# Kernel optimization log

Measured on AMD Instinct MI355X. Metric: run time of the kernel, lower is better.

The kernel has to match this reference:

```python
import jax, jax.numpy as jnp
import numpy as np

D_MODEL = 1024
D_HEAD = 64
B, S = 4, 4096


def setup_inputs() -> dict:
    key = jax.random.key(0)
    ks = jax.random.split(key, 7)
    inv = 1.0 / np.sqrt(D_MODEL)
    return {
        "x": jax.random.normal(ks[0], (B, S, D_MODEL), dtype=jnp.float32),
        "W_q": jax.random.normal(ks[1], (D_MODEL, D_HEAD), dtype=jnp.float32) * inv,
        "b_q": jax.random.normal(ks[2], (D_HEAD,), dtype=jnp.float32) * 0.02,
        "W_k": jax.random.normal(ks[3], (D_MODEL, D_HEAD), dtype=jnp.float32) * inv,
        "b_k": jax.random.normal(ks[4], (D_HEAD,), dtype=jnp.float32) * 0.02,
        "W_v": jax.random.normal(ks[5], (D_MODEL, D_HEAD), dtype=jnp.float32) * inv,
        "b_v": jax.random.normal(ks[6], (D_HEAD,), dtype=jnp.float32) * 0.02,
    }


def reference(x, W_q, b_q, W_k, b_k, W_v, b_v):
    # Projections: [B, S, d_head]
    Q = jnp.einsum("bsd,dh->bsh", x, W_q) + b_q
    K = jnp.einsum("bsd,dh->bsh", x, W_k) + b_k
    V = jnp.einsum("bsd,dh->bsh", x, W_v) + b_v
    scale = 1.0 / jnp.sqrt(jnp.asarray(Q.shape[-1], dtype=Q.dtype))
    scores = jnp.einsum("bqh,bkh->bqk", Q, K) * scale  # [B, S, S]
    seq_len = x.shape[1]
    causal = jnp.tril(jnp.ones((seq_len, seq_len), dtype=bool))
    scores = jnp.where(causal, scores, jnp.asarray(-jnp.inf, dtype=scores.dtype))
    A = jax.nn.softmax(scores, axis=-1)
    return jnp.einsum("bqk,bkh->bqh", A, V)  # [B, S, d_head]
```

## Files before the change

kernel.cpp:

```cpp
#include <hip/hip_runtime.h>

typedef __attribute__((ext_vector_type(4))) float f32x4;
typedef __attribute__((ext_vector_type(8))) short short8;
typedef unsigned short ushort_t;

constexpr int DM = 1024, DH = 64, S = 4096, B = 4;
constexpr float QSCALE = 0.125f * 1.44269504088896340736f;
constexpr int SPLIT = 4;

constexpr size_t WBT_OFF = 0;
constexpr size_t QB_OFF  = 393216;
constexpr size_t KB_OFF  = QB_OFF + 2097152;
constexpr size_t VT_OFF  = KB_OFF + 2097152;
constexpr size_t ML_OFF  = VT_OFF + 2097152;
constexpr size_t PO_OFF  = ML_OFF + 524288;

__device__ __forceinline__ ushort_t f2bf(float f) {
    unsigned u = __float_as_uint(f);
    u += 0x7FFFu + ((u >> 16) & 1u);
    return (ushort_t)(u >> 16);
}

__device__ __forceinline__ unsigned cvt_pk_bf16(float lo, float hi) {
    unsigned r;
    asm volatile("v_cvt_pk_bf16_f32 %0, %1, %2" : "=v"(r) : "v"(lo), "v"(hi));
    return r;
}

__device__ __forceinline__ void gl_lds16(const void* g, void* l) {
    __builtin_amdgcn_global_load_lds(
        (const __attribute__((address_space(1))) unsigned int*)g,
        (__attribute__((address_space(3))) unsigned int*)l, 16, 0, 0);
}

__global__ __launch_bounds__(256) void prep_w_kernel(
    const float* __restrict__ Wq, const float* __restrict__ Wk,
    const float* __restrict__ Wv, ushort_t* __restrict__ wbt)
{
    const int n = blockIdx.x;
    const int p = n >> 6, d = n & 63;
    const float* W = (p == 0) ? Wq : (p == 1) ? Wk : Wv;
    const int k0 = threadIdx.x * 4;
    ushort4 pack;
    pack.x = f2bf(W[(k0 + 0) * DH + d]);
    pack.y = f2bf(W[(k0 + 1) * DH + d]);
    pack.z = f2bf(W[(k0 + 2) * DH + d]);
    pack.w = f2bf(W[(k0 + 3) * DH + d]);
    *reinterpret_cast<ushort4*>(wbt + (size_t)n * DM + k0) = pack;
}

__global__ __launch_bounds__(512, 4) void qkv_mfma_kernel(
    const float* __restrict__ x, const ushort_t* __restrict__ wbt,
    const float* __restrict__ bq, const float* __restrict__ bk,
    const float* __restrict__ bv,
    ushort_t* __restrict__ qb, ushort_t* __restrict__ kb, ushort_t* __restrict__ vt)
{
    __shared__ uint4 AsU[2][256];
    __shared__ uint4 BsU[2][768];

    const int tid = threadIdx.x;
    const int wid = tid >> 6, lane = tid & 63;
    const int q16 = lane & 15, lg = lane >> 4;
    const int sub = wid & 1, np = wid >> 1;
    const int r0 = blockIdx.x * 32;
    const char* xB = (const char*)x;
    const char* wB = (const char*)wbt;

    auto task = [&](int tk, int buf, int kk) {
        if (tk < 4) {
            gl_lds16(xB + (size_t)(r0 + tk * 8 + (lane >> 3)) * 4096 + kk * 4
                        + (((lane & 7) ^ (lane >> 3)) << 4),
                     (char*)&AsU[buf][0] + tk * 1024 + lane * 16);
        } else {
            const int sg = tk - 4;
            gl_lds16(wB + (size_t)(sg * 16 + (lane >> 2)) * 2048 + kk * 2
                        + ((((lane & 3) ^ ((lane >> 2) & 3))) << 4),
                     (char*)&BsU[buf][0] + sg * 1024 + lane * 16);
        }
    };

    f32x4 acc[3];
#pragma unroll
    for (int j = 0; j < 3; ++j) acc[j] = {0.f, 0.f, 0.f, 0.f};

    task(2 * wid, 0, 0);
    task(2 * wid + 1, 0, 0);
    __syncthreads();

    const int row = sub * 16 + q16;
    for (int s = 0; s < 32; ++s) {
        const int buf = s & 1;
        if (s + 1 < 32) {
            task(2 * wid, buf ^ 1, (s + 1) * 32);
            task(2 * wid + 1, buf ^ 1, (s + 1) * 32);
        }
        const char* AsC = (const char*)&AsU[buf][0];
        const char* BsC = (const char*)&BsU[buf][0];
        const f32x4 a0 = *(const f32x4*)(AsC + row * 128 + (((2 * lg) ^ (row & 7)) << 4));
        const f32x4 a1 = *(const f32x4*)(AsC + row * 128 + (((2 * lg + 1) ^ (row & 7)) << 4));
        short8 Af;
        Af[0] = (short)f2bf(a0[0]); Af[1] = (short)f2bf(a0[1]);
        Af[2] = (short)f2bf(a0[2]); Af[3] = (short)f2bf(a0[3]);
        Af[4] = (short)f2bf(a1[0]); Af[5] = (short)f2bf(a1[1]);
        Af[6] = (short)f2bf(a1[2]); Af[7] = (short)f2bf(a1[3]);
        __builtin_amdgcn_s_setprio(1);
#pragma unroll
        for (int j = 0; j < 3; ++j) {
            const int nt = np * 3 + j;
            const short8 Bf = *(const short8*)(
                BsC + (nt * 16 + q16) * 64 + ((lg ^ (q16 & 3)) << 4));
            acc[j] = __builtin_amdgcn_mfma_f32_16x16x32_bf16(Af, Bf, acc[j], 0, 0, 0);
        }
        __builtin_amdgcn_s_setprio(0);
        __syncthreads();
    }

#pragma unroll
    for (int j = 0; j < 3; ++j) {
        const int nt = np * 3 + j;
        const int p = nt >> 2, d = ((nt & 3) << 4) + q16;
        const float* bp = (p == 0) ? bq : (p == 1) ? bk : bv;
        const float bb = bp[d];
#pragma unroll
        for (int r = 0; r < 4; ++r) {
            const int m = r0 + sub * 16 + (lg << 2) + r;
            const float v = acc[j][r] + bb;
            if (p == 0) {
                qb[(size_t)m * 64 + d] = f2bf(v * QSCALE);
            } else if (p == 1) {
                kb[(size_t)m * 64 + d] = f2bf(v);
            } else {
                const int bb_ = m >> 12, sx = m & 4095;
                vt[(size_t)bb_ * 262144 + (size_t)d * 4096 + sx] = f2bf(v);
            }
        }
    }
}

__global__ __launch_bounds__(256, 4) void attn_mfma_kernel(
    const ushort_t* __restrict__ qb, const ushort_t* __restrict__ kb,
    const ushort_t* __restrict__ vt, ushort_t* __restrict__ po,
    float* __restrict__ ml)
{
    __shared__ uint4 LsU[2][2048];
    __shared__ uint4 PsU[4][256];

    const int tid = threadIdx.x;
    const int wid = tid >> 6, lane = tid & 63;
    const int q16 = lane & 15, lg = lane >> 4;
    const int z = blockIdx.y;

    const int linear = blockIdx.x;
    const int xcd = linear & 7, idx = linear >> 3;
    const int b = xcd >> 1;
    const int qt = 63 - (idx * 2 + (xcd & 1));

    const int qrow = qt * 64 + wid * 16 + q16;
    const ushort_t* Qb = qb + (size_t)b * S * 64;
    const char* KbB = (const char*)(kb + (size_t)b * S * 64);
    const char* VtB = (const char*)(vt + (size_t)b * 64 * S);

    const short8 qf0 = *(const short8*)(Qb + (size_t)qrow * 64 + lg * 8);
    const short8 qf1 = *(const short8*)(Qb + (size_t)qrow * 64 + 32 + lg * 8);

    f32x4 o[4];
#pragma unroll
    for (int nt = 0; nt < 4; ++nt) o[nt] = {0.f, 0.f, 0.f, 0.f};
    float m = -1e30f, l = 0.f;

    char* PsC = (char*)&PsU[wid][0];
    const int ntiles = (qt >> 1) + 1;

    auto stage = [&](int t, int buf) {
        const int kv0 = t * 128;
#pragma unroll
        for (int i = 0; i < 8; ++i) {
            const int slot = i * 256 + tid;
            char* dst = (char*)&LsU[buf][0] + slot * 16;
            if (slot < 1024) {
                const int row = slot >> 3, ch = slot & 7;
                gl_lds16(KbB + (size_t)(kv0 + row) * 128 + ((ch ^ (row & 7)) << 4), dst);
            } else {
                const int s2 = slot - 1024;
                const int d = s2 >> 4, ch = s2 & 15;
                gl_lds16(VtB + (size_t)d * (S * 2) + kv0 * 2 + ((ch ^ (d & 15)) << 4), dst);
            }
        }
    };

    int buf = 0;
    if (z < ntiles) stage(z, 0);
    __syncthreads();

    for (int t = z; t < ntiles; t += SPLIT) {
        if (t + SPLIT < ntiles) stage(t + SPLIT, buf ^ 1);
        const char* KsC = (const char*)&LsU[buf][0];
        const char* VsC = KsC + 16384;
        const int kv0 = t * 128;

        f32x4 st[8];
#pragma unroll
        for (int mt = 0; mt < 8; ++mt) st[mt] = {0.f, 0.f, 0.f, 0.f};
#pragma unroll
        for (int ks = 0; ks < 2; ++ks) {
#pragma unroll
            for (int mg = 0; mg < 2; ++mg) {
                short8 kf[4];
#pragma unroll
                for (int j = 0; j < 4; ++j) {
                    const int mt = mg * 4 + j;
                    kf[j] = *(const short8*)(
                        KsC + (mt * 16 + q16) * 128 + (((lg + 4 * ks) ^ (q16 & 7)) << 4));
                }
                __builtin_amdgcn_s_setprio(1);
#pragma unroll
                for (int j = 0; j < 4; ++j)
                    st[mg * 4 + j] = __builtin_amdgcn_mfma_f32_16x16x32_bf16(
                        kf[j], (ks ? qf1 : qf0), st[mg * 4 + j], 0, 0, 0);
                __builtin_amdgcn_s_setprio(0);
            }
        }

        if (t == ntiles - 1) {
#pragma unroll
            for (int mt = 0; mt < 8; ++mt)
#pragma unroll
                for (int r = 0; r < 4; ++r)
                    if (kv0 + mt * 16 + (lg << 2) + r > qrow) st[mt][r] = -1e30f;
        }

        float tm = -1e30f;
#pragma unroll
        for (int mt = 0; mt < 8; ++mt)
#pragma unroll
            for (int r = 0; r < 4; ++r) tm = fmaxf(tm, st[mt][r]);
        tm = fmaxf(tm, __shfl_xor(tm, 16));
        tm = fmaxf(tm, __shfl_xor(tm, 32));

        if (__all(tm <= m)) {
            float ps = 0.f;
#pragma unroll
            for (int mt = 0; mt < 8; ++mt)
#pragma unroll
                for (int r = 0; r < 4; ++r) {
                    const float pv = exp2f(st[mt][r] - m);
                    st[mt][r] = pv;
                    ps += pv;
                }
            ps += __shfl_xor(ps, 16);
            ps += __shfl_xor(ps, 32);
            l += ps;
        } else {
            const float mn = fmaxf(m, tm);
            const float corr = exp2f(m - mn);
            float ps = 0.f;
#pragma unroll
            for (int mt = 0; mt < 8; ++mt)
#pragma unroll
                for (int r = 0; r < 4; ++r) {
                    const float pv = exp2f(st[mt][r] - mn);
                    st[mt][r] = pv;
                    ps += pv;
                }
            ps += __shfl_xor(ps, 16);
            ps += __shfl_xor(ps, 32);
            l = l * corr + ps;
            m = mn;
            float corr_row[4];
#pragma unroll
            for (int r = 0; r < 4; ++r) corr_row[r] = __shfl(corr, (lg << 2) | r);
#pragma unroll
            for (int nt = 0; nt < 4; ++nt)
#pragma unroll
                for (int r = 0; r < 4; ++r) o[nt][r] *= corr_row[r];
        }

#pragma unroll
        for (int mt = 0; mt < 8; ++mt) {
            uint2 w;
            w.x = cvt_pk_bf16(st[mt][0], st[mt][1]);
            w.y = cvt_pk_bf16(st[mt][2], st[mt][3]);
            const int ch = (2 * mt + (lg >> 1)) ^ q16;
            *reinterpret_cast<uint2*>(PsC + q16 * 256 + ch * 16 + (lg & 1) * 8) = w;
        }

        __builtin_amdgcn_s_setprio(1);
#pragma unroll
        for (int ks = 0; ks < 4; ++ks) {
            const short8 pa = *reinterpret_cast<const short8*>(
                PsC + q16 * 256 + (((4 * ks + lg) ^ q16) << 4));
#pragma unroll
            for (int nt = 0; nt < 4; ++nt) {
                const short8 vf = *(const short8*)(
                    VsC + (nt * 16 + q16) * 256 + (((ks * 4 + lg) ^ q16) << 4));
                o[nt] = __builtin_amdgcn_mfma_f32_16x16x32_bf16(pa, vf, o[nt], 0, 0, 0);
            }
        }
        __builtin_amdgcn_s_setprio(0);

        __syncthreads();
        buf ^= 1;
    }

    const int rowbase = qt * 64 + wid * 16;
    const size_t zb = (size_t)z * B * S + (size_t)b * S;
#pragma unroll
    for (int nt = 0; nt < 4; ++nt)
#pragma unroll
        for (int r = 0; r < 4; ++r)
            po[(zb + rowbase + (lg << 2) + r) * 64 + nt * 16 + q16] = f2bf(o[nt][r]);
    if (lg == 0) {
        ml[(zb + rowbase + q16) * 2 + 0] = m;
        ml[(zb + rowbase + q16) * 2 + 1] = l;
    }
}

__global__ __launch_bounds__(256) void merge_kernel(
    const ushort_t* __restrict__ po, const float* __restrict__ ml,
    float* __restrict__ out)
{
    const int idx = blockIdx.x * 256 + threadIdx.x;
    const int row = idx >> 3, c8 = idx & 7;

    float mv[SPLIT], lv[SPLIT];
#pragma unroll
    for (int zz = 0; zz < SPLIT; ++zz) {
        const float2 t = *(const float2*)(ml + ((size_t)zz * B * S + row) * 2);
        mv[zz] = t.x; lv[zz] = t.y;
    }
    const float mm = fmaxf(fmaxf(mv[0], mv[1]), fmaxf(mv[2], mv[3]));
    float L = 0.f, cz[SPLIT];
#pragma unroll
    for (int zz = 0; zz < SPLIT; ++zz) { cz[zz] = exp2f(mv[zz] - mm); L += lv[zz] * cz[zz]; }
    const float inv = 1.0f / L;

    float acc[8];
#pragma unroll
    for (int e = 0; e < 8; ++e) acc[e] = 0.f;
#pragma unroll
    for (int zz = 0; zz < SPLIT; ++zz) {
        const uint4 pk = *(const uint4*)(po + ((size_t)zz * B * S + row) * 64 + c8 * 8);
        const unsigned w[4] = {pk.x, pk.y, pk.z, pk.w};
#pragma unroll
        for (int i = 0; i < 4; ++i) {
            acc[2 * i + 0] += cz[zz] * __uint_as_float((w[i] & 0xFFFFu) << 16);
            acc[2 * i + 1] += cz[zz] * __uint_as_float((w[i] >> 16) << 16);
        }
    }
    float4 o0 = make_float4(acc[0] * inv, acc[1] * inv, acc[2] * inv, acc[3] * inv);
    float4 o1 = make_float4(acc[4] * inv, acc[5] * inv, acc[6] * inv, acc[7] * inv);
    *(float4*)(out + (size_t)row * 64 + c8 * 8 + 0) = o0;
    *(float4*)(out + (size_t)row * 64 + c8 * 8 + 4) = o1;
}

extern "C" void kernel_launch(void* const* d_in, const int* in_sizes, int n_in,
                              void* d_out, int out_size, void* d_ws, size_t ws_size,
                              hipStream_t stream) {
    const float* x  = (const float*)d_in[0];
    const float* Wq = (const float*)d_in[1];
    const float* bq = (const float*)d_in[2];
    const float* Wk = (const float*)d_in[3];
    const float* bk = (const float*)d_in[4];
    const float* Wv = (const float*)d_in[5];
    const float* bv = (const float*)d_in[6];
    float* out = (float*)d_out;

    char* ws = (char*)d_ws;
    ushort_t* wbt = (ushort_t*)(ws + WBT_OFF);
    ushort_t* qbp = (ushort_t*)(ws + QB_OFF);
    ushort_t* kbp = (ushort_t*)(ws + KB_OFF);
    ushort_t* vtp = (ushort_t*)(ws + VT_OFF);
    float*    mlp = (float*)(ws + ML_OFF);
    ushort_t* pop = (ushort_t*)(ws + PO_OFF);

    hipLaunchKernelGGL(prep_w_kernel, dim3(192), dim3(256), 0, stream, Wq, Wk, Wv, wbt);
    hipLaunchKernelGGL(qkv_mfma_kernel, dim3(512), dim3(512), 0, stream,
                       x, wbt, bq, bk, bv, qbp, kbp, vtp);
    hipLaunchKernelGGL(attn_mfma_kernel, dim3(256, SPLIT), dim3(256), 0, stream,
                       qbp, kbp, vtp, pop, mlp);
    hipLaunchKernelGGL(merge_kernel, dim3(512), dim3(256), 0, stream, pop, mlp, out);
}
```

Baseline: 72.78 us.

## Load x directly in QKV, single-buffer attention KV staging, software bf16 pack

The QKV projection now loads x rows straight from global memory into registers and only stages W through LDS, using 256-thread blocks over 16 rows each. The attention kernel drops double-buffered K/V staging for a single LDS buffer loaded synchronously before each tile, halving its K/V LDS use. The inline v_cvt_pk_bf16 asm is replaced with the software rounding routine. This trades load/compute overlap and a cheap conversion for lower LDS use and simpler code.

```diff
diff --git a/kernel.cpp b/kernel.cpp
--- a/kernel.cpp
+++ b/kernel.cpp
@@ -19,12 +19,6 @@
     unsigned u = __float_as_uint(f);
     u += 0x7FFFu + ((u >> 16) & 1u);
     return (ushort_t)(u >> 16);
-}
-
-__device__ __forceinline__ unsigned cvt_pk_bf16(float lo, float hi) {
-    unsigned r;
-    asm volatile("v_cvt_pk_bf16_f32 %0, %1, %2" : "=v"(r) : "v"(lo), "v"(hi));
-    return r;
 }
 
 __device__ __forceinline__ void gl_lds16(const void* g, void* l) {
@@ -49,30 +43,27 @@
     *reinterpret_cast<ushort4*>(wbt + (size_t)n * DM + k0) = pack;
 }
 
-__global__ __launch_bounds__(512, 4) void qkv_mfma_kernel(
+__global__ __launch_bounds__(256, 4) void qkv_mfma_kernel(
     const float* __restrict__ x, const ushort_t* __restrict__ wbt,
     const float* __restrict__ bq, const float* __restrict__ bk,
     const float* __restrict__ bv,
     ushort_t* __restrict__ qb, ushort_t* __restrict__ kb, ushort_t* __restrict__ vt)
 {
-    __shared__ uint4 AsU[2][256];
     __shared__ uint4 BsU[2][768];
 
     const int tid = threadIdx.x;
     const int wid = tid >> 6, lane = tid & 63;
     const int q16 = lane & 15, lg = lane >> 4;
-    const int sub = wid & 1, np = wid >> 1;
-    const int r0 = blockIdx.x * 32;
-    const char* xB = (const char*)x;
+    const int np = wid;
+    const int r0 = blockIdx.x * 16;
     const char* wB = (const char*)wbt;
 
-    auto task = [&](int tk, int buf, int kk) {
-        if (tk < 4) {
-            gl_lds16(xB + (size_t)(r0 + tk * 8 + (lane >> 3)) * 4096 + kk * 4
-                        + (((lane & 7) ^ (lane >> 3)) << 4),
-                     (char*)&AsU[buf][0] + tk * 1024 + lane * 16);
-        } else {
-            const int sg = tk - 4;
+    const float* xr = x + (size_t)(r0 + q16) * DM + lg * 8;
+
+    auto stageB = [&](int kk, int buf) {
+#pragma unroll
+        for (int j = 0; j < 3; ++j) {
+            const int sg = np * 3 + j;
             gl_lds16(wB + (size_t)(sg * 16 + (lane >> 2)) * 2048 + kk * 2
                         + ((((lane & 3) ^ ((lane >> 2) & 3))) << 4),
                      (char*)&BsU[buf][0] + sg * 1024 + lane * 16);
@@ -83,26 +74,20 @@
 #pragma unroll
     for (int j = 0; j < 3; ++j) acc[j] = {0.f, 0.f, 0.f, 0.f};
 
-    task(2 * wid, 0, 0);
-    task(2 * wid + 1, 0, 0);
+    stageB(0, 0);
     __syncthreads();
 
-    const int row = sub * 16 + q16;
     for (int s = 0; s < 32; ++s) {
         const int buf = s & 1;
-        if (s + 1 < 32) {
-            task(2 * wid, buf ^ 1, (s + 1) * 32);
-            task(2 * wid + 1, buf ^ 1, (s + 1) * 32);
-        }
-        const char* AsC = (const char*)&AsU[buf][0];
+        if (s + 1 < 32) stageB((s + 1) * 32, buf ^ 1);
+        const float4 a0 = *(const float4*)(xr + s * 32);
+        const float4 a1 = *(const float4*)(xr + s * 32 + 4);
+        short8 Af;
+        Af[0] = (short)f2bf(a0.x); Af[1] = (short)f2bf(a0.y);
+        Af[2] = (short)f2bf(a0.z); Af[3] = (short)f2bf(a0.w);
+        Af[4] = (short)f2bf(a1.x); Af[5] = (short)f2bf(a1.y);
+        Af[6] = (short)f2bf(a1.z); Af[7] = (short)f2bf(a1.w);
         const char* BsC = (const char*)&BsU[buf][0];
-        const f32x4 a0 = *(const f32x4*)(AsC + row * 128 + (((2 * lg) ^ (row & 7)) << 4));
-        const f32x4 a1 = *(const f32x4*)(AsC + row * 128 + (((2 * lg + 1) ^ (row & 7)) << 4));
-        short8 Af;
-        Af[0] = (short)f2bf(a0[0]); Af[1] = (short)f2bf(a0[1]);
-        Af[2] = (short)f2bf(a0[2]); Af[3] = (short)f2bf(a0[3]);
-        Af[4] = (short)f2bf(a1[0]); Af[5] = (short)f2bf(a1[1]);
-        Af[6] = (short)f2bf(a1[2]); Af[7] = (short)f2bf(a1[3]);
         __builtin_amdgcn_s_setprio(1);
 #pragma unroll
         for (int j = 0; j < 3; ++j) {
@@ -123,7 +108,7 @@
         const float bb = bp[d];
 #pragma unroll
         for (int r = 0; r < 4; ++r) {
-            const int m = r0 + sub * 16 + (lg << 2) + r;
+            const int m = r0 + (lg << 2) + r;
             const float v = acc[j][r] + bb;
             if (p == 0) {
                 qb[(size_t)m * 64 + d] = f2bf(v * QSCALE);
@@ -142,7 +127,7 @@
     const ushort_t* __restrict__ vt, ushort_t* __restrict__ po,
     float* __restrict__ ml)
 {
-    __shared__ uint4 LsU[2][2048];
+    __shared__ uint4 LsU[2048];
     __shared__ uint4 PsU[4][256];
 
     const int tid = threadIdx.x;
@@ -171,12 +156,12 @@
     char* PsC = (char*)&PsU[wid][0];
     const int ntiles = (qt >> 1) + 1;
 
-    auto stage = [&](int t, int buf) {
+    auto stage = [&](int t) {
         const int kv0 = t * 128;
 #pragma unroll
         for (int i = 0; i < 8; ++i) {
             const int slot = i * 256 + tid;
-            char* dst = (char*)&LsU[buf][0] + slot * 16;
+            char* dst = (char*)&LsU[0] + slot * 16;
             if (slot < 1024) {
                 const int row = slot >> 3, ch = slot & 7;
                 gl_lds16(KbB + (size_t)(kv0 + row) * 128 + ((ch ^ (row & 7)) << 4), dst);
@@ -188,13 +173,10 @@
         }
     };
 
-    int buf = 0;
-    if (z < ntiles) stage(z, 0);
-    __syncthreads();
-
     for (int t = z; t < ntiles; t += SPLIT) {
-        if (t + SPLIT < ntiles) stage(t + SPLIT, buf ^ 1);
-        const char* KsC = (const char*)&LsU[buf][0];
+        stage(t);
+        __syncthreads();
+        const char* KsC = (const char*)&LsU[0];
         const char* VsC = KsC + 16384;
         const int kv0 = t * 128;
 
@@ -278,8 +260,8 @@
 #pragma unroll
         for (int mt = 0; mt < 8; ++mt) {
             uint2 w;
-            w.x = cvt_pk_bf16(st[mt][0], st[mt][1]);
-            w.y = cvt_pk_bf16(st[mt][2], st[mt][3]);
+            w.x = (unsigned)f2bf(st[mt][0]) | ((unsigned)f2bf(st[mt][1]) << 16);
+            w.y = (unsigned)f2bf(st[mt][2]) | ((unsigned)f2bf(st[mt][3]) << 16);
             const int ch = (2 * mt + (lg >> 1)) ^ q16;
             *reinterpret_cast<uint2*>(PsC + q16 * 256 + ch * 16 + (lg & 1) * 8) = w;
         }
@@ -299,7 +281,6 @@
         __builtin_amdgcn_s_setprio(0);
 
         __syncthreads();
-        buf ^= 1;
     }
 
     const int rowbase = qt * 64 + wid * 16;
@@ -374,7 +355,7 @@
     ushort_t* pop = (ushort_t*)(ws + PO_OFF);
 
     hipLaunchKernelGGL(prep_w_kernel, dim3(192), dim3(256), 0, stream, Wq, Wk, Wv, wbt);
-    hipLaunchKernelGGL(qkv_mfma_kernel, dim3(512), dim3(512), 0, stream,
+    hipLaunchKernelGGL(qkv_mfma_kernel, dim3(1024), dim3(256), 0, stream,
                        x, wbt, bq, bk, bv, qbp, kbp, vtp);
     hipLaunchKernelGGL(attn_mfma_kernel, dim3(256, SPLIT), dim3(256), 0, stream,
                        qbp, kbp, vtp, pop, mlp);
```

New measurement: 103.7 us. 42.5% more time.
